# Kernel tuning notes

Hardware: AMD Instinct MI355X
Metric: run time of the kernel (lower is better)

Reference implementation:

```python
import jax, jax.numpy as jnp
import numpy as np

B, N, F, D, H, K, L = 16, 2048, 40, 256, 8, 256, 4
DH = D // H  # 32

def setup_inputs() -> dict:
    key = jax.random.key(0)
    ks = jax.random.split(key, 12)
    rn = lambda k, shp: jax.random.normal(k, shp, dtype=jnp.float32) * 0.02
    return dict(
        x=jax.random.normal(ks[0], (B, N, F), dtype=jnp.float32),
        W_emb=rn(ks[1], (F, D)), b_emb=jnp.zeros((D,), jnp.float32),
        pos=rn(ks[11], (1, N, D)),
        ln0_g=jnp.ones((D,), jnp.float32), ln0_b=jnp.zeros((D,), jnp.float32),
        ln1_g=jnp.ones((L, D), jnp.float32), ln1_b=jnp.zeros((L, D), jnp.float32),
        Wq=rn(ks[2], (L, D, D)), Wk=rn(ks[3], (L, D, D)), Wv=rn(ks[4], (L, D, D)),
        Ek=rn(ks[5], (L, N, K)), Ev=rn(ks[6], (L, N, K)),
        Wo=rn(ks[7], (L, D, D)), bo=jnp.zeros((L, D), jnp.float32),
        ln2_g=jnp.ones((L, D), jnp.float32), ln2_b=jnp.zeros((L, D), jnp.float32),
        W1=rn(ks[8], (L, D, 4 * D)), b1=jnp.zeros((L, 4 * D), jnp.float32),
        W2=rn(ks[9], (L, 4 * D, D)), b2=jnp.zeros((L, D), jnp.float32),
        W_out=rn(ks[10], (D, 1)), b_out=jnp.zeros((1,), jnp.float32))

def _ln(t, g, b, eps=1e-5):
    m = t.mean(-1, keepdims=True)
    v = ((t - m) ** 2).mean(-1, keepdims=True)
    return (t - m) * jax.lax.rsqrt(v + eps) * g + b

def reference(x, W_emb, b_emb, pos, ln0_g, ln0_b, ln1_g, ln1_b, Wq, Wk, Wv,
              Ek, Ev, Wo, bo, ln2_g, ln2_b, W1, b1, W2, b2, W_out, b_out):
    h = x @ W_emb + b_emb + pos          # [B,N,D] embed + learned pos enc
    h = _ln(h, ln0_g, ln0_b)
    scale = DH ** -0.5
    for i in range(L):  # Linformer layer: prenorm attn + prenorm FF, residual
        a = _ln(h, ln1_g[i], ln1_b[i])
        q = (a @ Wq[i]).reshape(B, N, H, DH).transpose(0, 2, 1, 3)            # bhnd
        k = jnp.einsum('bnd,nk->bkd', a @ Wk[i], Ek[i])                        # low-rank proj
        v = jnp.einsum('bnd,nk->bkd', a @ Wv[i], Ev[i])
        k = k.reshape(B, K, H, DH).transpose(0, 2, 1, 3)                       # bhkd
        v = v.reshape(B, K, H, DH).transpose(0, 2, 1, 3)
        attn = jax.nn.softmax(jnp.einsum('bhnd,bhkd->bhnk', q, k) * scale, axis=-1)
        o = jnp.einsum('bhnk,bhkd->bhnd', attn, v).transpose(0, 2, 1, 3).reshape(B, N, D)
        h = h + o @ Wo[i] + bo[i]
        a = _ln(h, ln2_g[i], ln2_b[i])
        h = h + jax.nn.gelu(a @ W1[i] + b1[i], approximate=False) @ W2[i] + b2[i]
    return h @ W_out + b_out             # [B,N,1]
```

## Files before the change

### kernel.cpp

```cpp
#include <hip/hip_runtime.h>
#include <hip/hip_bf16.h>


typedef short bf16x8 __attribute__((ext_vector_type(8)));
typedef float f32x4 __attribute__((ext_vector_type(4)));
typedef unsigned int u32x4 __attribute__((ext_vector_type(4)));

#define GLOBAL_AS __attribute__((address_space(1)))
#define LDS_AS __attribute__((address_space(3)))

static __device__ __forceinline__ float gelu_f(float v) {
    const float u2 = v * (0.7978845608028654f + 0.03567740814183427f * v * v);
    const float t = 1.0f - 2.0f / (__expf(2.0f * u2) + 1.0f);
    return 0.5f * v * (1.0f + t);
}
static __device__ __forceinline__ ushort f2bf(float x) {
    __hip_bfloat16 h = __float2bfloat16(x);
    return __builtin_bit_cast(ushort, h);
}
static __device__ __forceinline__ float bf2f(ushort u) {
    unsigned int x = ((unsigned int)u) << 16;
    return __builtin_bit_cast(float, x);
}

__global__ __launch_bounds__(256)
void embed_ln3(const float* __restrict__ x, const float* __restrict__ Wemb,
               const float* __restrict__ bemb, const float* __restrict__ pos,
               const float* __restrict__ g0, const float* __restrict__ b0,
               ushort* __restrict__ H)
{
    __shared__ float xs[32][40];
    const int t = threadIdx.x, w = t >> 6, l = t & 63;
    const long row0 = (long)blockIdx.x * 32;
    for (int idx = t; idx < 32 * 40; idx += 256)
        ((float*)xs)[idx] = x[row0 * 40 + idx];
    __syncthreads();

    const int r0 = w * 8;
    const int nbase = (int)((row0 + r0) & 2047);
    const float4 be = *(const float4*)&bemb[l * 4];
    float4 acc[8];
    #pragma unroll 8
    for (int j = 0; j < 8; ++j) {
        const float4 pv = *(const float4*)&pos[(long)(nbase + j) * 256 + l * 4];
        acc[j].x = be.x + pv.x; acc[j].y = be.y + pv.y;
        acc[j].z = be.z + pv.z; acc[j].w = be.w + pv.w;
    }
    for (int f = 0; f < 40; ++f) {
        const float4 wv = *(const float4*)&Wemb[f * 256 + l * 4];
        #pragma unroll 8
        for (int j = 0; j < 8; ++j) {
            const float xf = xs[r0 + j][f];
            acc[j].x += xf * wv.x; acc[j].y += xf * wv.y;
            acc[j].z += xf * wv.z; acc[j].w += xf * wv.w;
        }
    }
    const float4 gv = *(const float4*)&g0[l * 4];
    const float4 bv = *(const float4*)&b0[l * 4];
    #pragma unroll 8
    for (int j = 0; j < 8; ++j) {
        float s = acc[j].x + acc[j].y + acc[j].z + acc[j].w;
        #pragma unroll
        for (int m = 32; m >= 1; m >>= 1) s += __shfl_xor(s, m);
        const float mean = s * (1.0f / 256.0f);
        const float dx = acc[j].x - mean, dy = acc[j].y - mean;
        const float dz = acc[j].z - mean, dw = acc[j].w - mean;
        float q = dx * dx + dy * dy + dz * dz + dw * dw;
        #pragma unroll
        for (int m = 32; m >= 1; m >>= 1) q += __shfl_xor(q, m);
        const float inv = rsqrtf(q * (1.0f / 256.0f) + 1e-5f);
        ushort4 y;
        y.x = f2bf(dx * inv * gv.x + bv.x);
        y.y = f2bf(dy * inv * gv.y + bv.y);
        y.z = f2bf(dz * inv * gv.z + bv.z);
        y.w = f2bf(dw * inv * gv.w + bv.w);
        *(ushort4*)&H[(row0 + r0 + j) * 256 + l * 4] = y;
    }
}

__global__ __launch_bounds__(256)
void ln_bf(const ushort* __restrict__ X, const float* __restrict__ g,
           const float* __restrict__ b, ushort* __restrict__ Y)
{
    const int row = blockIdx.x * 4 + (threadIdx.x >> 6);
    const int lane = threadIdx.x & 63;
    const long base = (long)row * 256 + lane * 4;
    const ushort4 xu = *(const ushort4*)&X[base];
    float4 xv;
    xv.x = bf2f(xu.x); xv.y = bf2f(xu.y); xv.z = bf2f(xu.z); xv.w = bf2f(xu.w);
    float s = xv.x + xv.y + xv.z + xv.w;
    #pragma unroll
    for (int m = 32; m >= 1; m >>= 1) s += __shfl_xor(s, m);
    const float mean = s * (1.0f / 256.0f);
    const float dx = xv.x - mean, dy = xv.y - mean, dz = xv.z - mean, dw = xv.w - mean;
    float q = dx * dx + dy * dy + dz * dz + dw * dw;
    #pragma unroll
    for (int m = 32; m >= 1; m >>= 1) q += __shfl_xor(q, m);
    const float inv = rsqrtf(q * (1.0f / 256.0f) + 1e-5f);
    const float4 gv = *(const float4*)&g[lane * 4];
    const float4 bv = *(const float4*)&b[lane * 4];
    ushort4 y;
    y.x = f2bf(dx * inv * gv.x + bv.x);
    y.y = f2bf(dy * inv * gv.y + bv.y);
    y.z = f2bf(dz * inv * gv.z + bv.z);
    y.w = f2bf(dw * inv * gv.w + bv.w);
    *(ushort4*)&Y[base] = y;
}

__global__ __launch_bounds__(256)
void ln_tr(const ushort* __restrict__ X, const float* __restrict__ g,
           const float* __restrict__ b, ushort* __restrict__ Y,
           ushort* __restrict__ aT)
{
    __shared__ ushort tile[32 * 258];
    const int t = threadIdx.x, w = t >> 6, l = t & 63;
    const long row0 = (long)blockIdx.x * 32;
    const float4 gv = *(const float4*)&g[l * 4];
    const float4 bv = *(const float4*)&b[l * 4];
    #pragma unroll 8
    for (int j = 0; j < 8; ++j) {
        const int r = w * 8 + j;
        const long base = (row0 + r) * 256 + l * 4;
        const ushort4 xu = *(const ushort4*)&X[base];
        float4 xv;
        xv.x = bf2f(xu.x); xv.y = bf2f(xu.y); xv.z = bf2f(xu.z); xv.w = bf2f(xu.w);
        float s = xv.x + xv.y + xv.z + xv.w;
        #pragma unroll
        for (int m = 32; m >= 1; m >>= 1) s += __shfl_xor(s, m);
        const float mean = s * (1.0f / 256.0f);
        const float dx = xv.x - mean, dy = xv.y - mean, dz = xv.z - mean, dw = xv.w - mean;
        float q = dx * dx + dy * dy + dz * dz + dw * dw;
        #pragma unroll
        for (int m = 32; m >= 1; m >>= 1) q += __shfl_xor(q, m);
        const float inv = rsqrtf(q * (1.0f / 256.0f) + 1e-5f);
        ushort4 y;
        y.x = f2bf(dx * inv * gv.x + bv.x);
        y.y = f2bf(dy * inv * gv.y + bv.y);
        y.z = f2bf(dz * inv * gv.z + bv.z);
        y.w = f2bf(dw * inv * gv.w + bv.w);
        *(ushort4*)&Y[base] = y;
        *(ushort4*)&tile[r * 258 + l * 4] = y;
    }
    __syncthreads();
    const int tx = t & 31, ty = t >> 5;
    const int b_ = (int)(row0 >> 11), nn = (int)(row0 & 2047);
    #pragma unroll 8
    for (int jj = 0; jj < 32; ++jj) {
        const int c = ty * 32 + jj;
        aT[((long)(b_ * 256 + c)) * 2048 + nn + tx] = tile[tx * 258 + c];
    }
}

__global__ __launch_bounds__(256)
void transpose_cast(const float* __restrict__ in, ushort* __restrict__ out,
                    int R, int C, long sIn, long sOut)
{
    __shared__ float tile[32][33];
    in += (long)blockIdx.z * sIn; out += (long)blockIdx.z * sOut;
    const int c0 = blockIdx.x * 32, r0 = blockIdx.y * 32;
    const int tx = threadIdx.x & 31, ty = threadIdx.x >> 5;
    #pragma unroll
    for (int j = 0; j < 4; ++j)
        tile[ty + j * 8][tx] = in[(long)(r0 + ty + j * 8) * C + c0 + tx];
    __syncthreads();
    #pragma unroll
    for (int j = 0; j < 4; ++j)
        out[(long)(c0 + ty + j * 8) * R + r0 + tx] = f2bf(tile[tx][ty + j * 8]);
}

template<int ACT, int HASB, int ACCF>
__global__ __launch_bounds__(256)
void gemm64(const ushort* __restrict__ A, const ushort* __restrict__ BT,
            const float* __restrict__ bias, ushort* __restrict__ Cout,
            int Kd, int lda, int ldb, int ldc,
            long sA, long sBT, long sC)
{
    __shared__ ushort Als[2][64 * 32];
    __shared__ ushort Bls[2][64 * 32];
    const int bz = blockIdx.z;
    const ushort* Ab = A + (long)bz * sA;
    const ushort* Bb = BT + (long)bz * sBT;
    const int m0 = blockIdx.x * 64, n0 = blockIdx.y * 64;
    const int t = threadIdx.x, l = t & 63, w = t >> 6;
    const int wr = w >> 1, wc = w & 1;
    const int fr = l & 15, fq = l >> 4;

    f32x4 acc[2][2];
    #pragma unroll
    for (int m = 0; m < 2; ++m)
        #pragma unroll
        for (int n = 0; n < 2; ++n) acc[m][n] = f32x4{0.f, 0.f, 0.f, 0.f};

    const int lrow_off = (l >> 2);
    const int lk_off = (((l & 3) ^ ((l >> 3) & 3)) * 8);
    const int c0c = 2 * w, c1c = 2 * w + 1;
    const int h0 = c0c >> 2, rb0 = (c0c & 3) * 16;
    const int h1 = c1c >> 2, rb1 = (c1c & 3) * 16;
    const ushort* Ag0 = Ab + (long)(m0 + rb0 + lrow_off) * lda + h0 * 32 + lk_off;
    const ushort* Ag1 = Ab + (long)(m0 + rb1 + lrow_off) * lda + h1 * 32 + lk_off;
    const ushort* Bg0 = Bb + (long)(n0 + rb0 + lrow_off) * ldb + h0 * 32 + lk_off;
    const ushort* Bg1 = Bb + (long)(n0 + rb1 + lrow_off) * ldb + h1 * 32 + lk_off;
    const int ad0 = rb0 * 32, ad1 = rb1 * 32;
    const int ks = ((fq ^ ((fr >> 1) & 3)) * 8);

    for (int kk = 0; kk < Kd; kk += 64) {
        __builtin_amdgcn_global_load_lds((const GLOBAL_AS void*)(Ag0 + kk),
                                         (LDS_AS void*)&Als[h0][ad0], 16, 0, 0);
        __builtin_amdgcn_global_load_lds((const GLOBAL_AS void*)(Ag1 + kk),
                                         (LDS_AS void*)&Als[h1][ad1], 16, 0, 0);
        __builtin_amdgcn_global_load_lds((const GLOBAL_AS void*)(Bg0 + kk),
                                         (LDS_AS void*)&Bls[h0][ad0], 16, 0, 0);
        __builtin_amdgcn_global_load_lds((const GLOBAL_AS void*)(Bg1 + kk),
                                         (LDS_AS void*)&Bls[h1][ad1], 16, 0, 0);
        __syncthreads();
        bf16x8 af[2][2], bfv[2][2];
        #pragma unroll
        for (int hh = 0; hh < 2; ++hh) {
            #pragma unroll
            for (int m = 0; m < 2; ++m)
                af[m][hh] = *(const bf16x8*)&Als[hh][(wr * 32 + m * 16 + fr) * 32 + ks];
            #pragma unroll
            for (int n = 0; n < 2; ++n)
                bfv[n][hh] = *(const bf16x8*)&Bls[hh][(wc * 32 + n * 16 + fr) * 32 + ks];
        }
        #pragma unroll
        for (int hh = 0; hh < 2; ++hh)
            #pragma unroll
            for (int m = 0; m < 2; ++m)
                #pragma unroll
                for (int n = 0; n < 2; ++n)
                    acc[m][n] = __builtin_amdgcn_mfma_f32_16x16x32_bf16(
                        af[m][hh], bfv[n][hh], acc[m][n], 0, 0, 0);
        __syncthreads();
    }

    float bsv[2];
    #pragma unroll
    for (int n = 0; n < 2; ++n) bsv[n] = HASB ? bias[n0 + wc * 32 + n * 16 + fr] : 0.f;
    ushort* Cp = Cout + (long)bz * sC;
    #pragma unroll
    for (int m = 0; m < 2; ++m) {
        #pragma unroll
        for (int r = 0; r < 4; ++r) {
            const int grow = m0 + wr * 32 + m * 16 + fq * 4 + r;
            const long rowoff = (long)grow * ldc + n0 + wc * 32 + fr;
            #pragma unroll
            for (int n = 0; n < 2; ++n) {
                float v = acc[m][n][r] + bsv[n];
                if (ACT) v = gelu_f(v);
                const long off = rowoff + n * 16;
                if (ACCF) v += bf2f(Cp[off]);
                Cp[off] = f2bf(v);
            }
        }
    }
}

__global__ __launch_bounds__(256)
void attn_mfma2(const ushort* __restrict__ Q, const ushort* __restrict__ Kp,
                const ushort* __restrict__ VpT, ushort* __restrict__ O)
{
    __shared__ ushort Kls[256 * 40];
    __shared__ ushort Vls[32 * 264];
    const int qt = blockIdx.x, h = blockIdx.y, b = blockIdx.z;
    const int n0 = qt * 64;
    const int t = threadIdx.x, w = t >> 6, l = t & 63;
    const int fr = l & 15, fq = l >> 4;

    #pragma unroll
    for (int it = 0; it < 4; ++it) {
        const int r = (t >> 2) + it * 64, c = (t & 3) * 8;
        *(float4*)&Kls[r * 40 + c] =
            *(const float4*)&Kp[((long)(b * 256 + r)) * 256 + h * 32 + c];
    }
    {
        const int r = t >> 3, c0 = (t & 7) * 32;
        const ushort* src = VpT + ((long)(b * 256 + h * 32 + r)) * 256 + c0;
        #pragma unroll
        for (int j = 0; j < 4; ++j)
            *(float4*)&Vls[r * 264 + c0 + j * 8] = *(const float4*)(src + j * 8);
    }
    const bf16x8 bq = *(const bf16x8*)
        &Q[((long)(b * 2048 + n0 + w * 16 + fr)) * 256 + h * 32 + fq * 8];
    __syncthreads();

    f32x4 s[16];
    #pragma unroll
    for (int n = 0; n < 16; ++n) {
        const bf16x8 ak = *(const bf16x8*)&Kls[(n * 16 + fr) * 40 + fq * 8];
        s[n] = __builtin_amdgcn_mfma_f32_16x16x32_bf16(ak, bq, f32x4{0.f,0.f,0.f,0.f}, 0, 0, 0);
    }
    const float scale = 0.17677669529663687f;
    float mx = -1e30f;
    #pragma unroll
    for (int n = 0; n < 16; ++n)
        #pragma unroll
        for (int r = 0; r < 4; ++r) { s[n][r] *= scale; mx = fmaxf(mx, s[n][r]); }
    mx = fmaxf(mx, __shfl_xor(mx, 16));
    mx = fmaxf(mx, __shfl_xor(mx, 32));
    float sm = 0.f;
    unsigned int p[16][2];
    #pragma unroll
    for (int n = 0; n < 16; ++n) {
        float e0 = __expf(s[n][0] - mx), e1 = __expf(s[n][1] - mx);
        float e2 = __expf(s[n][2] - mx), e3 = __expf(s[n][3] - mx);
        sm += (e0 + e1) + (e2 + e3);
        p[n][0] = ((unsigned int)f2bf(e1) << 16) | f2bf(e0);
        p[n][1] = ((unsigned int)f2bf(e3) << 16) | f2bf(e2);
    }
    sm += __shfl_xor(sm, 16);
    sm += __shfl_xor(sm, 32);

    const int fqa = fq & 1, fqb = fq >> 1;
    f32x4 o[2] = {f32x4{0.f,0.f,0.f,0.f}, f32x4{0.f,0.f,0.f,0.f}};
    #pragma unroll
    for (int kk = 0; kk < 8; ++kk) {
        u32x4 bw;
        #pragma unroll
        for (int wd = 0; wd < 4; ++wd) {
            const int srcl = fr + ((2 * fqa + (wd >> 1)) << 4);
            const unsigned int v0 = __shfl((int)p[2 * kk][wd & 1], srcl);
            const unsigned int v1 = __shfl((int)p[2 * kk + 1][wd & 1], srcl);
            bw[wd] = fqb ? v1 : v0;
        }
        const bf16x8 breg = __builtin_bit_cast(bf16x8, bw);
        #pragma unroll
        for (int nd = 0; nd < 2; ++nd) {
            const bf16x8 av = *(const bf16x8*)&Vls[(nd * 16 + fr) * 264 + kk * 32 + fq * 8];
            o[nd] = __builtin_amdgcn_mfma_f32_16x16x32_bf16(av, breg, o[nd], 0, 0, 0);
        }
    }
    const float inv = 1.0f / sm;
    const long rowbase = ((long)(b * 2048 + n0 + w * 16 + fr)) * 256 + h * 32;
    #pragma unroll
    for (int nd = 0; nd < 2; ++nd) {
        ushort4 y;
        y.x = f2bf(o[nd][0] * inv); y.y = f2bf(o[nd][1] * inv);
        y.z = f2bf(o[nd][2] * inv); y.w = f2bf(o[nd][3] * inv);
        *(ushort4*)&O[rowbase + nd * 16 + fq * 4] = y;
    }
}

__global__ __launch_bounds__(256)
void out_kernel(const ushort* __restrict__ H, const float* __restrict__ Wout,
                const float* __restrict__ bout, float* __restrict__ out)
{
    const int row = blockIdx.x * 4 + (threadIdx.x >> 6);
    const int lane = threadIdx.x & 63;
    const ushort4 hu = *(const ushort4*)&H[(long)row * 256 + lane * 4];
    float4 wv = *(const float4*)&Wout[lane * 4];
    float s = bf2f(hu.x) * wv.x + bf2f(hu.y) * wv.y +
              bf2f(hu.z) * wv.z + bf2f(hu.w) * wv.w;
    #pragma unroll
    for (int m = 32; m >= 1; m >>= 1) s += __shfl_xor(s, m);
    if (lane == 0) out[row] = s + bout[0];
}

extern "C" void kernel_launch(void* const* d_in, const int* in_sizes, int n_in,
                              void* d_out, int out_size, void* d_ws, size_t ws_size,
                              hipStream_t stream)
{
    const float* x    = (const float*)d_in[0];
    const float* Wemb = (const float*)d_in[1];
    const float* bemb = (const float*)d_in[2];
    const float* pos  = (const float*)d_in[3];
    const float* ln0g = (const float*)d_in[4];
    const float* ln0b = (const float*)d_in[5];
    const float* ln1g = (const float*)d_in[6];
    const float* ln1b = (const float*)d_in[7];
    const float* Wq   = (const float*)d_in[8];
    const float* Wk   = (const float*)d_in[9];
    const float* Wv   = (const float*)d_in[10];
    const float* Ek   = (const float*)d_in[11];
    const float* Ev   = (const float*)d_in[12];
    const float* Wo   = (const float*)d_in[13];
    const float* bo   = (const float*)d_in[14];
    const float* ln2g = (const float*)d_in[15];
    const float* ln2b = (const float*)d_in[16];
    const float* W1   = (const float*)d_in[17];
    const float* b1   = (const float*)d_in[18];
    const float* W2   = (const float*)d_in[19];
    const float* b2   = (const float*)d_in[20];
    const float* Wout = (const float*)d_in[21];
    const float* bout = (const float*)d_in[22];

    char* ws = (char*)d_ws;
    ushort* h    = (ushort*)(ws + 0);
    ushort* abf  = (ushort*)(ws + 33554432L);
    ushort* aT   = (ushort*)(ws + 50331648L);
    ushort* kp   = (ushort*)(ws + 67108864L);
    ushort* vpT  = (ushort*)(ws + 69206016L);
    ushort* apkv = (ushort*)(ws + 71303168L);
    ushort* qbf  = (ushort*)(ws + 100663296L);
    ushort* hid  = (ushort*)(ws + 50331648L);
    ushort* WT   = (ushort*)(ws + 117440512L);
    ushort* WqT  = WT;
    ushort* WkT  = WT + 262144;
    ushort* WvT  = WT + 524288;
    ushort* WoT  = WT + 786432;
    ushort* W1T  = WT + 1048576;
    ushort* W2T  = WT + 2097152;
    ushort* EkvT = WT + 3145728;
    float* outp = (float*)d_out;

    transpose_cast<<<dim3(8, 8, 4), 256, 0, stream>>>(Wq, WqT, 256, 256, 65536, 65536);
    transpose_cast<<<dim3(8, 8, 4), 256, 0, stream>>>(Wk, WkT, 256, 256, 65536, 65536);
    transpose_cast<<<dim3(8, 8, 4), 256, 0, stream>>>(Wv, WvT, 256, 256, 65536, 65536);
    transpose_cast<<<dim3(8, 8, 4), 256, 0, stream>>>(Wo, WoT, 256, 256, 65536, 65536);
    transpose_cast<<<dim3(32, 8, 4), 256, 0, stream>>>(W1, W1T, 256, 1024, 262144, 262144);
    transpose_cast<<<dim3(8, 32, 4), 256, 0, stream>>>(W2, W2T, 1024, 256, 262144, 262144);
    transpose_cast<<<dim3(8, 64, 4), 256, 0, stream>>>(Ek, EkvT, 2048, 256, 524288, 1048576);
    transpose_cast<<<dim3(8, 64, 4), 256, 0, stream>>>(Ev, EkvT + 524288, 2048, 256, 524288, 1048576);

    embed_ln3<<<1024, 256, 0, stream>>>(x, Wemb, bemb, pos, ln0g, ln0b, h);
    ln_tr<<<1024, 256, 0, stream>>>(h, ln1g, ln1b, abf, aT);

    for (int i = 0; i < 4; ++i) {
        const ushort* WqT_i = WqT + i * 65536;
        const ushort* WkT_i = WkT + i * 65536;
        const ushort* WvT_i = WvT + i * 65536;
        const ushort* WoT_i = WoT + i * 65536;
        const ushort* W1T_i = W1T + i * 262144;
        const ushort* W2T_i = W2T + i * 262144;
        const ushort* EkvT_i = EkvT + (long)i * 1048576;

        gemm64<0,0,0><<<dim3(512, 4, 1), 256, 0, stream>>>(abf, WqT_i, nullptr, qbf,
            256, 256, 256, 256, 0, 0, 0);
        gemm64<0,0,0><<<dim3(8, 4, 16), 256, 0, stream>>>(EkvT_i, aT, nullptr, apkv,
            2048, 2048, 2048, 256, 0, 524288, 131072);
        gemm64<0,0,0><<<dim3(4, 4, 16), 256, 0, stream>>>(apkv, WkT_i, nullptr, kp,
            256, 256, 256, 256, 131072, 0, 65536);
        gemm64<0,0,0><<<dim3(4, 4, 16), 256, 0, stream>>>(WvT_i, apkv + 65536, nullptr, vpT,
            256, 256, 256, 256, 0, 131072, 65536);
        attn_mfma2<<<dim3(32, 8, 16), 256, 0, stream>>>(qbf, kp, vpT, abf);
        gemm64<0,1,1><<<dim3(512, 4, 1), 256, 0, stream>>>(abf, WoT_i, bo + i * 256, h,
            256, 256, 256, 256, 0, 0, 0);
        ln_bf<<<8192, 256, 0, stream>>>(h, ln2g + i * 256, ln2b + i * 256, abf);
        gemm64<1,1,0><<<dim3(512, 16, 1), 256, 0, stream>>>(abf, W1T_i,
            b1 + (long)i * 1024, hid, 256, 256, 256, 1024, 0, 0, 0);
        gemm64<0,1,1><<<dim3(512, 4, 1), 256, 0, stream>>>(hid, W2T_i, b2 + i * 256, h,
            1024, 1024, 1024, 256, 0, 0, 0);
        if (i < 3)
            ln_tr<<<1024, 256, 0, stream>>>(h, ln1g + (i + 1) * 256,
                ln1b + (i + 1) * 256, abf, aT);
    }
    out_kernel<<<8192, 256, 0, stream>>>(h, Wout, bout, outp);
}
```

Before: 812.0 us.

## Give each wave private LDS tiles in gemm64 to drop block barriers

```diff
diff --git a/kernel.cpp b/kernel.cpp
--- a/kernel.cpp
+++ b/kernel.cpp
@@ -175,8 +175,8 @@
             int Kd, int lda, int ldb, int ldc,
             long sA, long sBT, long sC)
 {
-    __shared__ ushort Als[2][64 * 32];
-    __shared__ ushort Bls[2][64 * 32];
+    __shared__ ushort Als[4][2][1024];
+    __shared__ ushort Bls[4][2][1024];
     const int bz = blockIdx.z;
     const ushort* Ab = A + (long)bz * sA;
     const ushort* Bb = BT + (long)bz * sBT;
@@ -191,37 +191,40 @@
         #pragma unroll
         for (int n = 0; n < 2; ++n) acc[m][n] = f32x4{0.f, 0.f, 0.f, 0.f};
 
-    const int lrow_off = (l >> 2);
-    const int lk_off = (((l & 3) ^ ((l >> 3) & 3)) * 8);
-    const int c0c = 2 * w, c1c = 2 * w + 1;
-    const int h0 = c0c >> 2, rb0 = (c0c & 3) * 16;
-    const int h1 = c1c >> 2, rb1 = (c1c & 3) * 16;
-    const ushort* Ag0 = Ab + (long)(m0 + rb0 + lrow_off) * lda + h0 * 32 + lk_off;
-    const ushort* Ag1 = Ab + (long)(m0 + rb1 + lrow_off) * lda + h1 * 32 + lk_off;
-    const ushort* Bg0 = Bb + (long)(n0 + rb0 + lrow_off) * ldb + h0 * 32 + lk_off;
-    const ushort* Bg1 = Bb + (long)(n0 + rb1 + lrow_off) * ldb + h1 * 32 + lk_off;
-    const int ad0 = rb0 * 32, ad1 = rb1 * 32;
+    const int lrow = l >> 2;
+    const int lslot = (((l & 3) ^ ((l >> 3) & 3)) * 8);
+    const ushort* Ag[2][2];
+    const ushort* Bg[2][2];
+    #pragma unroll
+    for (int hh = 0; hh < 2; ++hh)
+        #pragma unroll
+        for (int c = 0; c < 2; ++c) {
+            Ag[hh][c] = Ab + (long)(m0 + wr * 32 + c * 16 + lrow) * lda + hh * 32 + lslot;
+            Bg[hh][c] = Bb + (long)(n0 + wc * 32 + c * 16 + lrow) * ldb + hh * 32 + lslot;
+        }
     const int ks = ((fq ^ ((fr >> 1) & 3)) * 8);
 
     for (int kk = 0; kk < Kd; kk += 64) {
-        __builtin_amdgcn_global_load_lds((const GLOBAL_AS void*)(Ag0 + kk),
-                                         (LDS_AS void*)&Als[h0][ad0], 16, 0, 0);
-        __builtin_amdgcn_global_load_lds((const GLOBAL_AS void*)(Ag1 + kk),
-                                         (LDS_AS void*)&Als[h1][ad1], 16, 0, 0);
-        __builtin_amdgcn_global_load_lds((const GLOBAL_AS void*)(Bg0 + kk),
-                                         (LDS_AS void*)&Bls[h0][ad0], 16, 0, 0);
-        __builtin_amdgcn_global_load_lds((const GLOBAL_AS void*)(Bg1 + kk),
-                                         (LDS_AS void*)&Bls[h1][ad1], 16, 0, 0);
-        __syncthreads();
+        #pragma unroll
+        for (int hh = 0; hh < 2; ++hh)
+            #pragma unroll
+            for (int c = 0; c < 2; ++c) {
+                __builtin_amdgcn_global_load_lds((const GLOBAL_AS void*)(Ag[hh][c] + kk),
+                                                 (LDS_AS void*)&Als[w][hh][c * 512], 16, 0, 0);
+                __builtin_amdgcn_global_load_lds((const GLOBAL_AS void*)(Bg[hh][c] + kk),
+                                                 (LDS_AS void*)&Bls[w][hh][c * 512], 16, 0, 0);
+            }
+        asm volatile("s_waitcnt vmcnt(0)" ::: "memory");
+        __builtin_amdgcn_sched_barrier(0);
         bf16x8 af[2][2], bfv[2][2];
         #pragma unroll
         for (int hh = 0; hh < 2; ++hh) {
             #pragma unroll
             for (int m = 0; m < 2; ++m)
-                af[m][hh] = *(const bf16x8*)&Als[hh][(wr * 32 + m * 16 + fr) * 32 + ks];
+                af[m][hh] = *(const bf16x8*)&Als[w][hh][(m * 16 + fr) * 32 + ks];
             #pragma unroll
             for (int n = 0; n < 2; ++n)
-                bfv[n][hh] = *(const bf16x8*)&Bls[hh][(wc * 32 + n * 16 + fr) * 32 + ks];
+                bfv[n][hh] = *(const bf16x8*)&Bls[w][hh][(n * 16 + fr) * 32 + ks];
         }
         #pragma unroll
         for (int hh = 0; hh < 2; ++hh)
@@ -231,7 +234,7 @@
                 for (int n = 0; n < 2; ++n)
                     acc[m][n] = __builtin_amdgcn_mfma_f32_16x16x32_bf16(
                         af[m][hh], bfv[n][hh], acc[m][n], 0, 0, 0);
-        __syncthreads();
+        __builtin_amdgcn_sched_barrier(0);
     }
 
     float bsv[2];
```

New measurement: 985.8 us. +21.4%, slower.
